# Performance work log

Measured on AMD Instinct MI355X. Metric: run time of the kernel, lower is better.

The kernel has to match this reference:

```python
import jax, jax.numpy as jnp
import numpy as np

NBITS = 8
REDUCE = 64
OUT = 512


def setup_inputs() -> dict:
    key = jax.random.key(0)
    ks = jax.random.split(key, 6)
    T, B, C = 512, 16, 512
    ne = 2 ** NBITS
    x = jax.random.normal(ks[0], (T, B, C), dtype=jnp.float32)
    key_in = jax.random.normal(ks[1], (T, B, C), dtype=jnp.float32)  # unused by forward (overwritten)
    # xavier-ish init scales
    map_w = jax.random.normal(ks[2], (NBITS, C), dtype=jnp.float32) * np.sqrt(2.0 / (C + NBITS))
    map_b = jnp.zeros((NBITS,), dtype=jnp.float32)
    pw_w1 = jax.random.normal(ks[3], (REDUCE, C), dtype=jnp.float32) * np.sqrt(2.0 / (C + REDUCE))
    pw_w21 = jax.random.normal(ks[4], (ne, OUT * REDUCE), dtype=jnp.float32) * np.sqrt(2.0 / (ne + OUT * REDUCE))
    pw_w22 = jax.random.normal(ks[5], (ne, OUT * REDUCE), dtype=jnp.float32) * np.sqrt(2.0 / (ne + OUT * REDUCE))
    pw_B = jnp.zeros((1, 1, OUT), dtype=jnp.float32)
    return {"x": x, "key": key_in, "map_w": map_w, "map_b": map_b,
            "pw_w1": pw_w1, "pw_w21": pw_w21, "pw_w22": pw_w22, "pw_B": pw_B}


def reference(x, key, map_w, map_b, pw_w1, pw_w21, pw_w22, pw_B):
    # x: (T,B,C). `key` arg is overwritten by x in the original source.
    T, B, C = x.shape
    nbits = map_w.shape[0]
    out_dim = pw_B.shape[-1]
    reduce_dim = pw_w1.shape[0]

    k = x.reshape(T * B, C) @ map_w.T + map_b          # (T*B, nbits)
    z = jnp.clip(1.2 * jax.nn.sigmoid(k) - 0.1, 0.0, 1.0)  # saturated sigmoid
    code = (z > 0.5).astype(z.dtype)                   # eval: hard binary code

    pows = (2 ** jnp.arange(nbits, dtype=jnp.int32))   # bit_to_int weights
    qz1 = jnp.sum(code.astype(jnp.int32) * pows, axis=-1)          # (T*B,)
    qz2 = jnp.sum((1 - code.astype(jnp.int32)) * pows, axis=-1)    # (T*B,)

    # gather per-token expert rows and synthesize per-token weight matrix
    w2 = (pw_w21[qz1] + pw_w22[qz2]).reshape(T, B, out_dim, reduce_dim)

    # original computes (w2 @ pw_w1) @ x; reassociated as w2 @ (pw_w1 @ x)
    # to avoid materializing the (T,B,out,in) intermediate (same math)
    v = jnp.einsum('ri,tbi->tbr', pw_w1, x)            # (T,B,reduce)
    y = jnp.einsum('tbor,tbr->tbo', w2, v) + pw_B      # (T,B,out)

    loss = jnp.zeros((1,), dtype=x.dtype)
    return (y, loss)
```

## Files before the change

kernel.cpp:

```cpp
#include <hip/hip_runtime.h>

#define NTOK 8192
#define CDIM 512
#define NB   8
#define RD   64
#define OD   512

#define TPB_A 8
#define XPAD  4
#define XROW  (CDIM + XPAD)
#define XROW4 (XROW / 4)

typedef unsigned char u8;

__device__ __forceinline__ float4 f4add(float4 a, float4 b) {
    return make_float4(a.x + b.x, a.y + b.y, a.z + b.z, a.w + b.w);
}

__global__ __launch_bounds__(128) void phaseA(
    const float* __restrict__ x, const float* __restrict__ map_w,
    const float* __restrict__ map_b, const float* __restrict__ w1,
    u8* __restrict__ q_out, float* __restrict__ v_out,
    float* __restrict__ loss_out)
{
    const int t    = threadIdx.x;
    const int tok0 = blockIdx.x * TPB_A;
    __shared__ __align__(16) float xs[TPB_A * XROW];

    const float4* xsrc = (const float4*)(x + (size_t)tok0 * CDIM);
    #pragma unroll
    for (int i = t; i < TPB_A * (CDIM / 4); i += 128) {
        int r = i >> 7, c = i & 127;
        *((float4*)(xs + r * XROW) + c) = xsrc[i];
    }
    __syncthreads();

    {
        const int bit  = t & 7;
        const int half = (t >> 3) & 1;
        const int tk   = t >> 4;
        const float4* m4 = (const float4*)(map_w + (size_t)bit * CDIM) + half * 64;
        const float4* x4 = (const float4*)xs + tk * XROW4 + half * 64;
        double a0 = 0.0, a1 = 0.0;
        for (int j = 0; j < 64; ++j) {
            float4 m = m4[j], xv = x4[j];
            a0 += (double)m.x * (double)xv.x + (double)m.y * (double)xv.y;
            a1 += (double)m.z * (double)xv.z + (double)m.w * (double)xv.w;
        }
        double a = a0 + a1;
        a += __shfl_xor(a, 8);
        const double k = a + (double)map_b[bit];
        const unsigned long long m = __ballot(k > 0.0);
        if ((t & 15) == 0) {
            int g = (t >> 4) & 3;
            q_out[tok0 + tk] = (u8)((m >> (g * 16)) & 0xFFull);
        }
    }

    {
        const int r  = t & 63;
        const int tg = t >> 6;
        const float4* w4 = (const float4*)(w1 + (size_t)r * CDIM);
        const float4* xb = (const float4*)xs + (size_t)(tg * 4) * XROW4;
        float acc0 = 0.f, acc1 = 0.f, acc2 = 0.f, acc3 = 0.f;
        for (int j = 0; j < CDIM / 4; ++j) {
            float4 wv = w4[j];
            float4 x0 = xb[j];
            float4 x1 = xb[XROW4 + j];
            float4 x2 = xb[2 * XROW4 + j];
            float4 x3 = xb[3 * XROW4 + j];
            acc0 += wv.x * x0.x + wv.y * x0.y + wv.z * x0.z + wv.w * x0.w;
            acc1 += wv.x * x1.x + wv.y * x1.y + wv.z * x1.z + wv.w * x1.w;
            acc2 += wv.x * x2.x + wv.y * x2.y + wv.z * x2.z + wv.w * x2.w;
            acc3 += wv.x * x3.x + wv.y * x3.y + wv.z * x3.z + wv.w * x3.w;
        }
        float* vo = v_out + (size_t)(tok0 + tg * 4) * RD + r;
        vo[0 * RD] = acc0; vo[1 * RD] = acc1; vo[2 * RD] = acc2; vo[3 * RD] = acc3;
    }

    if (blockIdx.x == 0 && t == 0) loss_out[0] = 0.0f;
}

__global__ __launch_bounds__(128) void phaseB(
    const u8* __restrict__ q_arr, const float* __restrict__ v_arr,
    const float* __restrict__ w21, const float* __restrict__ w22,
    const float* __restrict__ pwB, float* __restrict__ y)
{
    const int q  = blockIdx.x >> 2;
    const int qu = blockIdx.x & 3;
    const int t  = threadIdx.x;
    const int o  = qu * 128 + t;

    __shared__ unsigned short list[NTOK];
    __shared__ int cnt;
    __shared__ __align__(16) float vs[8 * RD];

    const float4* pa = (const float4*)w21 + (size_t)q * (OD * RD / 4) + (size_t)o * (RD / 4);
    const float4* pb = (const float4*)w22 + (size_t)(255 - q) * (OD * RD / 4) + (size_t)o * (RD / 4);
    float4 a0 = pa[0],  a1 = pa[1],  a2 = pa[2],  a3 = pa[3],
           a4 = pa[4],  a5 = pa[5],  a6 = pa[6],  a7 = pa[7],
           a8 = pa[8],  a9 = pa[9],  a10 = pa[10], a11 = pa[11],
           a12 = pa[12], a13 = pa[13], a14 = pa[14], a15 = pa[15];
    float4 b0 = pb[0],  b1 = pb[1],  b2 = pb[2],  b3 = pb[3],
           b4 = pb[4],  b5 = pb[5],  b6 = pb[6],  b7 = pb[7],
           b8 = pb[8],  b9 = pb[9],  b10 = pb[10], b11 = pb[11],
           b12 = pb[12], b13 = pb[13], b14 = pb[14], b15 = pb[15];

    if (t == 0) cnt = 0;
    __syncthreads();

    const uint4* qa = (const uint4*)q_arr;
    for (int i = t; i < NTOK / 16; i += 128) {
        uint4 u = qa[i];
        int sbase = i * 16;
#define CHK(WORD, OFF) { unsigned uw = (WORD); \
        if ((int)(uw & 0xFFu)         == q) list[atomicAdd(&cnt, 1)] = (unsigned short)(sbase + (OFF));     \
        if ((int)((uw >> 8)  & 0xFFu) == q) list[atomicAdd(&cnt, 1)] = (unsigned short)(sbase + (OFF) + 1); \
        if ((int)((uw >> 16) & 0xFFu) == q) list[atomicAdd(&cnt, 1)] = (unsigned short)(sbase + (OFF) + 2); \
        if ((int)(uw >> 24)           == q) list[atomicAdd(&cnt, 1)] = (unsigned short)(sbase + (OFF) + 3); }
        CHK(u.x, 0) CHK(u.y, 4) CHK(u.z, 8) CHK(u.w, 12)
#undef CHK
    }
    __syncthreads();
    const int n = cnt;
    if (n == 0) return;

    float4 w0 = f4add(a0, b0),  w1 = f4add(a1, b1),  w2 = f4add(a2, b2),  w3 = f4add(a3, b3),
           w4 = f4add(a4, b4),  w5 = f4add(a5, b5),  w6 = f4add(a6, b6),  w7 = f4add(a7, b7),
           w8 = f4add(a8, b8),  w9 = f4add(a9, b9),  w10 = f4add(a10, b10), w11 = f4add(a11, b11),
           w12 = f4add(a12, b12), w13 = f4add(a13, b13), w14 = f4add(a14, b14), w15 = f4add(a15, b15);
    const float bias = pwB[o];

    const float4* v4 = (const float4*)v_arr;
    for (int base = 0; base < n; base += 8) {
        const int nb = min(8, n - base);
        if (t < nb * 16)
            ((float4*)vs)[t] = v4[(size_t)list[base + (t >> 4)] * (RD / 4) + (t & 15)];
        __syncthreads();
        int i = 0;
        for (; i + 2 <= nb; i += 2) {
            const float4* p0 = (const float4*)vs + (size_t)i * 16;
            const float4* p1 = p0 + 16;
            float acc0 = bias, acc1 = bias;
#define STEP(J, W) { float4 u0 = p0[J], u1 = p1[J]; \
            acc0 += W.x * u0.x + W.y * u0.y + W.z * u0.z + W.w * u0.w; \
            acc1 += W.x * u1.x + W.y * u1.y + W.z * u1.z + W.w * u1.w; }
            STEP(0, w0)  STEP(1, w1)  STEP(2, w2)  STEP(3, w3)
            STEP(4, w4)  STEP(5, w5)  STEP(6, w6)  STEP(7, w7)
            STEP(8, w8)  STEP(9, w9)  STEP(10, w10) STEP(11, w11)
            STEP(12, w12) STEP(13, w13) STEP(14, w14) STEP(15, w15)
#undef STEP
            y[(size_t)list[base + i]     * OD + o] = acc0;
            y[(size_t)list[base + i + 1] * OD + o] = acc1;
        }
        if (i < nb) {
            const float4* p0 = (const float4*)vs + (size_t)i * 16;
            float acc0 = bias;
#define STEP1(J, W) { float4 u0 = p0[J]; \
            acc0 += W.x * u0.x + W.y * u0.y + W.z * u0.z + W.w * u0.w; }
            STEP1(0, w0)  STEP1(1, w1)  STEP1(2, w2)  STEP1(3, w3)
            STEP1(4, w4)  STEP1(5, w5)  STEP1(6, w6)  STEP1(7, w7)
            STEP1(8, w8)  STEP1(9, w9)  STEP1(10, w10) STEP1(11, w11)
            STEP1(12, w12) STEP1(13, w13) STEP1(14, w14) STEP1(15, w15)
#undef STEP1
            y[(size_t)list[base + i] * OD + o] = acc0;
        }
        __syncthreads();
    }
}

__global__ __launch_bounds__(256) void mono(
    const float* __restrict__ x, const float* __restrict__ map_w,
    const float* __restrict__ map_b, const float* __restrict__ w1,
    const float* __restrict__ w21, const float* __restrict__ w22,
    const float* __restrict__ pwB, float* __restrict__ y)
{
    const int tok = blockIdx.x;
    const int t   = threadIdx.x;
    __shared__ float xsh[CDIM];
    __shared__ float vsh[RD];
    __shared__ int qsh;

    if (t == 0) qsh = 0;
    for (int i = t; i < CDIM; i += 256) xsh[i] = x[(size_t)tok * CDIM + i];
    __syncthreads();

    if (t < NB) {
        double a = 0.0;
        const float* mrow = map_w + (size_t)t * CDIM;
        for (int j = 0; j < CDIM; ++j) a += (double)mrow[j] * (double)xsh[j];
        a += (double)map_b[t];
        if (a > 0.0) atomicOr(&qsh, 1 << t);
    }
    if (t < RD) {
        const float* wrow = w1 + (size_t)t * CDIM;
        float acc = 0.f;
        for (int j = 0; j < CDIM; ++j) acc += wrow[j] * xsh[j];
        vsh[t] = acc;
    }
    __syncthreads();

    const int q = qsh;
    for (int o = t; o < OD; o += 256) {
        const float* pa = w21 + (size_t)q * (OD * RD) + (size_t)o * RD;
        const float* pb = w22 + (size_t)(255 - q) * (OD * RD) + (size_t)o * RD;
        float acc = pwB[o];
        for (int r = 0; r < RD; ++r) acc += (pa[r] + pb[r]) * vsh[r];
        y[(size_t)tok * OD + o] = acc;
    }
    if (tok == 0 && t == 0) y[(size_t)NTOK * OD] = 0.0f;
}

extern "C" void kernel_launch(void* const* d_in, const int* in_sizes, int n_in,
                              void* d_out, int out_size, void* d_ws, size_t ws_size,
                              hipStream_t stream) {
    const float* x     = (const float*)d_in[0];
    const float* map_w = (const float*)d_in[2];
    const float* map_b = (const float*)d_in[3];
    const float* w1    = (const float*)d_in[4];
    const float* w21   = (const float*)d_in[5];
    const float* w22   = (const float*)d_in[6];
    const float* pwB   = (const float*)d_in[7];
    float* out = (float*)d_out;

    const size_t need = (size_t)NTOK + (size_t)NTOK * RD * sizeof(float);
    if (ws_size >= need) {
        u8*    q_ws = (u8*)d_ws;
        float* v_ws = (float*)((char*)d_ws + NTOK);
        phaseA<<<NTOK / TPB_A, 128, 0, stream>>>(x, map_w, map_b, w1, q_ws, v_ws,
                                                 out + (size_t)NTOK * OD);
        phaseB<<<256 * 4, 128, 0, stream>>>(q_ws, v_ws, w21, w22, pwB, out);
    } else {
        mono<<<NTOK, 256, 0, stream>>>(x, map_w, map_b, w1, w21, w22, pwB, out);
    }
}
```

Baseline: 198.5 us.

## Double tokens per block in phaseA, prefetch codes and weights, add occupancy hints

PhaseA now handles 16 tokens per block. Each thread computes 8 token accumulators per weight row, so every w1 load is reused across more tokens, and w1 loads are software-prefetched in two register banks. The hash-bit projection is restructured so one thread computes a full 512-length dot product per bit, which removes the cross-lane shuffle. PhaseB issues its code-array loads up front, before the expert-weight gathers and the barrier, to overlap their latency, and both kernels get a min-blocks launch-bounds hint.

```diff
diff --git a/kernel.cpp b/kernel.cpp
--- a/kernel.cpp
+++ b/kernel.cpp
@@ -6,7 +6,7 @@
 #define RD   64
 #define OD   512
 
-#define TPB_A 8
+#define TPB_A 16
 #define XPAD  4
 #define XROW  (CDIM + XPAD)
 #define XROW4 (XROW / 4)
@@ -16,8 +16,11 @@
 __device__ __forceinline__ float4 f4add(float4 a, float4 b) {
     return make_float4(a.x + b.x, a.y + b.y, a.z + b.z, a.w + b.w);
 }
-
-__global__ __launch_bounds__(128) void phaseA(
+__device__ __forceinline__ float dot4(float4 a, float4 b) {
+    return a.x * b.x + a.y * b.y + a.z * b.z + a.w * b.w;
+}
+
+__global__ __launch_bounds__(128, 2) void phaseA(
     const float* __restrict__ x, const float* __restrict__ map_w,
     const float* __restrict__ map_b, const float* __restrict__ w1,
     u8* __restrict__ q_out, float* __restrict__ v_out,
@@ -36,24 +39,21 @@
     __syncthreads();
 
     {
-        const int bit  = t & 7;
-        const int half = (t >> 3) & 1;
-        const int tk   = t >> 4;
-        const float4* m4 = (const float4*)(map_w + (size_t)bit * CDIM) + half * 64;
-        const float4* x4 = (const float4*)xs + tk * XROW4 + half * 64;
+        const int bit = t & 7, tk = t >> 3;
+        const float4* m4 = (const float4*)(map_w + (size_t)bit * CDIM);
+        const float4* x4 = (const float4*)xs + tk * XROW4;
         double a0 = 0.0, a1 = 0.0;
-        for (int j = 0; j < 64; ++j) {
+        for (int j = 0; j < CDIM / 4; ++j) {
             float4 m = m4[j], xv = x4[j];
             a0 += (double)m.x * (double)xv.x + (double)m.y * (double)xv.y;
             a1 += (double)m.z * (double)xv.z + (double)m.w * (double)xv.w;
         }
-        double a = a0 + a1;
-        a += __shfl_xor(a, 8);
-        const double k = a + (double)map_b[bit];
-        const unsigned long long m = __ballot(k > 0.0);
-        if ((t & 15) == 0) {
-            int g = (t >> 4) & 3;
-            q_out[tok0 + tk] = (u8)((m >> (g * 16)) & 0xFFull);
+        double k = a0 + a1 + (double)map_b[bit];
+        unsigned long long m = __ballot(k > 0.0);
+        const int lane = t & 63;
+        if ((lane & 7) == 0) {
+            int g = lane >> 3;
+            q_out[tok0 + tk] = (u8)((m >> (g * 8)) & 0xFFull);
         }
     }
 
@@ -61,27 +61,43 @@
         const int r  = t & 63;
         const int tg = t >> 6;
         const float4* w4 = (const float4*)(w1 + (size_t)r * CDIM);
-        const float4* xb = (const float4*)xs + (size_t)(tg * 4) * XROW4;
+        const float4* xq = (const float4*)xs + (size_t)(tg * 8) * XROW4;
         float acc0 = 0.f, acc1 = 0.f, acc2 = 0.f, acc3 = 0.f;
-        for (int j = 0; j < CDIM / 4; ++j) {
-            float4 wv = w4[j];
-            float4 x0 = xb[j];
-            float4 x1 = xb[XROW4 + j];
-            float4 x2 = xb[2 * XROW4 + j];
-            float4 x3 = xb[3 * XROW4 + j];
-            acc0 += wv.x * x0.x + wv.y * x0.y + wv.z * x0.z + wv.w * x0.w;
-            acc1 += wv.x * x1.x + wv.y * x1.y + wv.z * x1.z + wv.w * x1.w;
-            acc2 += wv.x * x2.x + wv.y * x2.y + wv.z * x2.z + wv.w * x2.w;
-            acc3 += wv.x * x3.x + wv.y * x3.y + wv.z * x3.z + wv.w * x3.w;
-        }
-        float* vo = v_out + (size_t)(tok0 + tg * 4) * RD + r;
+        float acc4 = 0.f, acc5 = 0.f, acc6 = 0.f, acc7 = 0.f;
+
+#define CONSUME(WV, J) { const int jj = (J);                       \
+        acc0 += dot4(WV, xq[jj]);                                  \
+        acc1 += dot4(WV, xq[1 * XROW4 + jj]);                      \
+        acc2 += dot4(WV, xq[2 * XROW4 + jj]);                      \
+        acc3 += dot4(WV, xq[3 * XROW4 + jj]);                      \
+        acc4 += dot4(WV, xq[4 * XROW4 + jj]);                      \
+        acc5 += dot4(WV, xq[5 * XROW4 + jj]);                      \
+        acc6 += dot4(WV, xq[6 * XROW4 + jj]);                      \
+        acc7 += dot4(WV, xq[7 * XROW4 + jj]); }
+
+        float4 A0 = w4[0], A1 = w4[1], A2 = w4[2], A3 = w4[3];
+        float4 B0, B1, B2, B3;
+        for (int b = 0; b < CDIM / 4; b += 8) {
+            B0 = w4[b + 4]; B1 = w4[b + 5]; B2 = w4[b + 6]; B3 = w4[b + 7];
+            CONSUME(A0, b)     CONSUME(A1, b + 1)
+            CONSUME(A2, b + 2) CONSUME(A3, b + 3)
+            if (b + 8 < CDIM / 4) {
+                A0 = w4[b + 8]; A1 = w4[b + 9]; A2 = w4[b + 10]; A3 = w4[b + 11];
+            }
+            CONSUME(B0, b + 4) CONSUME(B1, b + 5)
+            CONSUME(B2, b + 6) CONSUME(B3, b + 7)
+        }
+#undef CONSUME
+
+        float* vo = v_out + (size_t)(tok0 + tg * 8) * RD + r;
         vo[0 * RD] = acc0; vo[1 * RD] = acc1; vo[2 * RD] = acc2; vo[3 * RD] = acc3;
+        vo[4 * RD] = acc4; vo[5 * RD] = acc5; vo[6 * RD] = acc6; vo[7 * RD] = acc7;
     }
 
     if (blockIdx.x == 0 && t == 0) loss_out[0] = 0.0f;
 }
 
-__global__ __launch_bounds__(128) void phaseB(
+__global__ __launch_bounds__(128, 2) void phaseB(
     const u8* __restrict__ q_arr, const float* __restrict__ v_arr,
     const float* __restrict__ w21, const float* __restrict__ w22,
     const float* __restrict__ pwB, float* __restrict__ y)
@@ -94,6 +110,9 @@
     __shared__ unsigned short list[NTOK];
     __shared__ int cnt;
     __shared__ __align__(16) float vs[8 * RD];
+
+    const uint4* qa = (const uint4*)q_arr;
+    uint4 qv0 = qa[t], qv1 = qa[t + 128], qv2 = qa[t + 256], qv3 = qa[t + 384];
 
     const float4* pa = (const float4*)w21 + (size_t)q * (OD * RD / 4) + (size_t)o * (RD / 4);
     const float4* pb = (const float4*)w22 + (size_t)(255 - q) * (OD * RD / 4) + (size_t)o * (RD / 4);
@@ -109,18 +128,16 @@
     if (t == 0) cnt = 0;
     __syncthreads();
 
-    const uint4* qa = (const uint4*)q_arr;
-    for (int i = t; i < NTOK / 16; i += 128) {
-        uint4 u = qa[i];
-        int sbase = i * 16;
-#define CHK(WORD, OFF) { unsigned uw = (WORD); \
-        if ((int)(uw & 0xFFu)         == q) list[atomicAdd(&cnt, 1)] = (unsigned short)(sbase + (OFF));     \
-        if ((int)((uw >> 8)  & 0xFFu) == q) list[atomicAdd(&cnt, 1)] = (unsigned short)(sbase + (OFF) + 1); \
-        if ((int)((uw >> 16) & 0xFFu) == q) list[atomicAdd(&cnt, 1)] = (unsigned short)(sbase + (OFF) + 2); \
-        if ((int)(uw >> 24)           == q) list[atomicAdd(&cnt, 1)] = (unsigned short)(sbase + (OFF) + 3); }
-        CHK(u.x, 0) CHK(u.y, 4) CHK(u.z, 8) CHK(u.w, 12)
+#define CHK(WORD, SB, OFF) { unsigned uw = (WORD); \
+    if ((int)(uw & 0xFFu)         == q) list[atomicAdd(&cnt, 1)] = (unsigned short)((SB) + (OFF));     \
+    if ((int)((uw >> 8)  & 0xFFu) == q) list[atomicAdd(&cnt, 1)] = (unsigned short)((SB) + (OFF) + 1); \
+    if ((int)((uw >> 16) & 0xFFu) == q) list[atomicAdd(&cnt, 1)] = (unsigned short)((SB) + (OFF) + 2); \
+    if ((int)(uw >> 24)           == q) list[atomicAdd(&cnt, 1)] = (unsigned short)((SB) + (OFF) + 3); }
+    { int sb = t * 16;          CHK(qv0.x, sb, 0) CHK(qv0.y, sb, 4) CHK(qv0.z, sb, 8) CHK(qv0.w, sb, 12) }
+    { int sb = (t + 128) * 16;  CHK(qv1.x, sb, 0) CHK(qv1.y, sb, 4) CHK(qv1.z, sb, 8) CHK(qv1.w, sb, 12) }
+    { int sb = (t + 256) * 16;  CHK(qv2.x, sb, 0) CHK(qv2.y, sb, 4) CHK(qv2.z, sb, 8) CHK(qv2.w, sb, 12) }
+    { int sb = (t + 384) * 16;  CHK(qv3.x, sb, 0) CHK(qv3.y, sb, 4) CHK(qv3.z, sb, 8) CHK(qv3.w, sb, 12) }
 #undef CHK
-    }
     __syncthreads();
     const int n = cnt;
     if (n == 0) return;
```

After: 198.1 us. Within noise of the previous version (-0.2%).
